# Kernel optimization log

Measured on AMD Instinct MI355X. Metric: run time of the kernel, lower is better.

The kernel has to match this reference:

```python
import jax, jax.numpy as jnp
import numpy as np

D = 128   # query_token_dim = tgt_token_dim = qk_dim = v_dim (code constraints)
NH = 8
HD = D // NH
SCALE = HD ** -0.5
B = 4096  # BH1W1: number of cost-map query locations
H0, W0 = 12, 18  # target token spatial size (H3, W3)


def _ln(x, g, b, eps=1e-5):
    m = x.mean(-1, keepdims=True)
    v = ((x - m) ** 2).mean(-1, keepdims=True)
    return (x - m) * jax.lax.rsqrt(v + eps) * g + b


def _broad_attn(q1, kw, vw):
    # q1: [D] single query broadcast across batch; kw, vw: [B, L, D]
    Bq, L, _ = kw.shape
    qh = q1.reshape(NH, HD)
    kh = kw.reshape(Bq, L, NH, HD)
    vh = vw.reshape(Bq, L, NH, HD)
    a = jax.nn.softmax(jnp.einsum('hd,blhd->bhl', qh, kh) * SCALE, axis=-1)
    return jnp.einsum('bhl,blhd->bhd', a, vh).reshape(Bq, D)


def _forward(query, tgt_token, ln1_g, ln1_b, ln2_g, ln2_b, wq, bq, wk, bk, wv, bv,
             wp, bp, f1w, f1b, f2w, f2b, cw, cb,
             ln1c_g, ln1c_b, ln2c_g, ln2c_b, wqc, bqc, wkc, bkc, wvc, bvc,
             wpc, bpc, f1cw, f1cb, f2cw, f2cb, H, W):
    Bq = tgt_token.shape[0]
    sc = query  # [1, 10, D]
    # ---- fine branch: 6 windows (2x3 grid) over full-res target tokens ----
    qn = _ln(query[:, :6, :], ln1_g, ln1_b)
    q = (qn @ wq + bq)[0]                                   # [6, D]
    k = (tgt_token @ wk + bk).reshape(Bq, H, W, D)
    v = (tgt_token @ wv + bv).reshape(Bq, H, W, D)
    hs = [(0, H // 2), (H // 2, H)]
    ws = [(0, W // 3), (W // 3, 2 * (W // 3)), (2 * (W // 3), W)]
    wins = [(h0, h1, w0, w1) for (h0, h1) in hs for (w0, w1) in ws]
    outs = [_broad_attn(q[i],
                        k[:, h0:h1, w0:w1].reshape(Bq, -1, D),
                        v[:, h0:h1, w0:w1].reshape(Bq, -1, D))
            for i, (h0, h1, w0, w1) in enumerate(wins)]
    x = jnp.stack(outs, axis=1)                             # [B, 6, D]
    x = sc[:, :6, :] + (x @ wp + bp)
    xn = _ln(x, ln2_g, ln2_b)
    x_fine = x + (jax.nn.gelu(xn @ f1w + f1b, approximate=False) @ f2w + f2b)
    # ---- coarse branch: 3x3/s2 conv downsample, 4 windows (2x2 grid) ----
    tc = jax.lax.conv_general_dilated(tgt_token.reshape(Bq, H, W, D), cw,
                                      (2, 2), ((1, 1), (1, 1)),
                                      dimension_numbers=('NHWC', 'HWIO', 'NHWC')) + cb
    Hc, Wc = tc.shape[1], tc.shape[2]
    qn = _ln(sc[:, 6:10, :], ln1c_g, ln1c_b)
    qc = (qn @ wqc + bqc)[0]                                # [4, D]
    kc = tc @ wkc + bkc
    vc = tc @ wvc + bvc
    hs = [(0, Hc // 2), (Hc // 2, Hc)]
    ws = [(0, Wc // 2), (Wc // 2, Wc)]
    wins = [(h0, h1, w0, w1) for (h0, h1) in hs for (w0, w1) in ws]
    outs = [_broad_attn(qc[i],
                        kc[:, h0:h1, w0:w1].reshape(Bq, -1, D),
                        vc[:, h0:h1, w0:w1].reshape(Bq, -1, D))
            for i, (h0, h1, w0, w1) in enumerate(wins)]
    x = jnp.stack(outs, axis=1)                             # [B, 4, D]
    x = sc[:, 6:10, :] + (x @ wpc + bpc)
    xn = _ln(x, ln2c_g, ln2c_b)
    x_coarse = x + (jax.nn.gelu(xn @ f1cw + f1cb, approximate=False) @ f2cw + f2cb)
    return jnp.concatenate([x_fine, x_coarse], axis=1)      # [B, 10, D]


def setup_inputs():
    key = jax.random.key(0)
    ks = jax.random.split(key, 16)
    def w(k, shape):
        return jax.random.normal(k, shape, jnp.float32) * 0.05
    z = jnp.zeros((D,), jnp.float32)
    o = jnp.ones((D,), jnp.float32)
    return dict(
        query=jax.random.normal(ks[0], (1, 10, D), jnp.float32),
        tgt_token=jax.random.normal(ks[1], (B, H0 * W0, D), jnp.float32),
        ln1_g=o, ln1_b=z, ln2_g=o, ln2_b=z,
        wq=w(ks[2], (D, D)), bq=z, wk=w(ks[3], (D, D)), bk=z,
        wv=w(ks[4], (D, D)), bv=z, wp=w(ks[5], (D, D)), bp=z,
        f1w=w(ks[6], (D, D)), f1b=z, f2w=w(ks[7], (D, D)), f2b=z,
        cw=w(ks[8], (3, 3, D, D)), cb=z,
        ln1c_g=o, ln1c_b=z, ln2c_g=o, ln2c_b=z,
        wqc=w(ks[9], (D, D)), bqc=z, wkc=w(ks[10], (D, D)), bkc=z,
        wvc=w(ks[11], (D, D)), bvc=z, wpc=w(ks[12], (D, D)), bpc=z,
        f1cw=w(ks[13], (D, D)), f1cb=z, f2cw=w(ks[14], (D, D)), f2cb=z,
        H=H0, W=W0,
    )


def reference(query, tgt_token, ln1_g, ln1_b, ln2_g, ln2_b, wq, bq, wk, bk, wv, bv,
              wp, bp, f1w, f1b, f2w, f2b, cw, cb,
              ln1c_g, ln1c_b, ln2c_g, ln2c_b, wqc, bqc, wkc, bkc, wvc, bvc,
              wpc, bpc, f1cw, f1cb, f2cw, f2cb, H, W):
    return _forward(query, tgt_token, ln1_g, ln1_b, ln2_g, ln2_b, wq, bq, wk, bk,
                    wv, bv, wp, bp, f1w, f1b, f2w, f2b, cw, cb,
                    ln1c_g, ln1c_b, ln2c_g, ln2c_b, wqc, bqc, wkc, bkc, wvc, bvc,
                    wpc, bpc, f1cw, f1cb, f2cw, f2cb, H, W)
```

## Files before the change

### kernel.cpp

```cpp
#include <hip/hip_runtime.h>
#include <math.h>


typedef short   mfrag  __attribute__((ext_vector_type(8)));
typedef float   floatx4 __attribute__((ext_vector_type(4)));
typedef unsigned short us4 __attribute__((ext_vector_type(4)));
typedef unsigned short us8 __attribute__((ext_vector_type(8)));
typedef unsigned int u32x4 __attribute__((ext_vector_type(4)));

#define LL   216
#define LC   54
#define TP1  136
#define TP2  72

__device__ __forceinline__ float b2f(unsigned short u){
  return __uint_as_float(((unsigned int)u) << 16);
}
__device__ __forceinline__ unsigned short f2b(float f){
  unsigned int x = __float_as_uint(f);
  return (unsigned short)((x + 0x7fffu + ((x >> 16) & 1u)) >> 16);
}
__device__ __forceinline__ floatx4 mfma16(mfrag a, mfrag b, floatx4 c){
  return __builtin_amdgcn_mfma_f32_16x16x32_bf16(a, b, c, 0, 0, 0);
}
__device__ __forceinline__ mfrag zfrag(){ mfrag z = {0,0,0,0,0,0,0,0}; return z; }

union F8 { unsigned short u[8]; mfrag v; };

struct Par {
  const float *query,*tgt,*ln1g,*ln1b,*ln2g,*ln2b,*wq,*bq,*wk,*wv,*bv,
              *wp,*bp,*f1w,*f1b,*f2w,*f2b,*cw,*cb;
  const float *ln1cg,*ln1cb,*ln2cg,*ln2cb,*wqc,*bqc,*wkc,*wvc,*bvc,
              *wpc,*bpc,*f1cw,*f1cb,*f2cw,*f2cb;
  unsigned short *U;
  float          *uc;
  float          *cvb;
  unsigned short *G;
  unsigned short *cwvT;
  unsigned short *wT;
  float          *out;
};

__global__ __launch_bounds__(256) void k0a(Par p){
  __shared__ float qn[10][128];
  __shared__ float qp[10][128];
  __shared__ unsigned short wkb[128*130];
  int tid = threadIdx.x;
  if (tid < 10){
    int r = tid;
    const float* row = p.query + r*128;
    float s1=0.f, s2=0.f;
    for (int c=0;c<128;c++){ float v=row[c]; s1+=v; s2+=v*v; }
    float m = s1/128.f, var = s2/128.f - m*m;
    float inv = rsqrtf(var + 1e-5f);
    const float* g  = (r<6)? p.ln1g : p.ln1cg;
    const float* bb = (r<6)? p.ln1b : p.ln1cb;
    for (int c=0;c<128;c++) qn[r][c] = (row[c]-m)*inv*g[c] + bb[c];
  }
  __syncthreads();
  for (int o=tid;o<1280;o+=256){
    int i=o>>7, d=o&127;
    const float* w  = (i<6)? p.wq : p.wqc;
    const float* bi = (i<6)? p.bq : p.bqc;
    float acc = bi[d];
    for (int c=0;c<128;c++) acc += qn[i][c]*w[c*128+d];
    qp[i][d]=acc;
  }
  if (tid < 128){
    int d = tid; float a = p.bvc[d];
    for (int c=0;c<128;c++) a += p.cb[c] * p.wvc[c*128+d];
    p.cvb[d] = a;
  }
  __syncthreads();
  for (int o=tid;o<16384;o+=256) wkb[(o>>7)*130 + (o&127)] = f2b(p.wk[o]);
  __syncthreads();
  for (int o=tid;o<6144;o+=256){
    int ih=o>>7, c=o&127, i=ih>>3, h=ih&7;
    float a=0.f;
    #pragma unroll
    for (int dd=0;dd<16;dd++) a += b2f(wkb[c*130 + h*16+dd]) * qp[i][h*16+dd];
    p.U[ih*128+c] = f2b(0.25f*a);
  }
  __syncthreads();
  for (int o=tid;o<16384;o+=256) wkb[(o>>7)*130 + (o&127)] = f2b(p.wkc[o]);
  __syncthreads();
  for (int o=tid;o<4096;o+=256){
    int ih=o>>7, c=o&127, i=ih>>3, h=ih&7;
    float a=0.f;
    #pragma unroll
    for (int dd=0;dd<16;dd++) a += b2f(wkb[c*130 + h*16+dd]) * qp[6+i][h*16+dd];
    p.uc[ih*128+c] = 0.25f*a;
  }
}

__global__ __launch_bounds__(256) void ktrans(Par p){
  __shared__ float lt[128*129];
  int bid = blockIdx.x, tid = threadIdx.x;
  const float* src;
  switch(bid){ case 0: src=p.wp;  break; case 1: src=p.f1w;  break;
               case 2: src=p.f2w; break; case 3: src=p.wpc;  break;
               case 4: src=p.f1cw;break; case 5: src=p.f2cw; break;
               case 6: src=p.wv;  break; default: src=p.wvc; }
  unsigned short* dst = p.wT + bid*16384;
  for (int o=tid;o<16384;o+=256){ int k=o>>7, n=o&127; lt[n*129+k] = src[o]; }
  __syncthreads();
  for (int o=tid;o<16384;o+=256){ int n=o>>7, k=o&127; dst[o] = f2b(lt[n*129+k]); }
}

__global__ __launch_bounds__(256) void kfold(Par p){
  __shared__ alignas(16) unsigned short cwb[128*136];
  __shared__ alignas(16) unsigned short ucb[32*136];
  int bid=blockIdx.x, tid=threadIdx.x;
  int lane=tid&63, w=tid>>6, q4=lane>>4, n16=lane&15;
  int tap = (bid<9)? bid : bid-9;
  for (int o=tid;o<16384;o+=256)
    cwb[(o>>7)*136 + (o&127)] = f2b(p.cw[(size_t)tap*16384 + o]);
  if (bid < 9){
    for (int o=tid;o<4096;o+=256) ucb[(o>>7)*136 + (o&127)] = f2b(p.uc[o]);
    __syncthreads();
    #pragma unroll
    for (int nt2=0;nt2<2;nt2++){
      int nt = w + nt2*4;
      #pragma unroll
      for (int mt=0;mt<2;mt++){
        floatx4 acc={0.f,0.f,0.f,0.f};
        #pragma unroll
        for (int ks=0;ks<4;ks++){
          mfrag a  = *reinterpret_cast<const mfrag*>(ucb + (mt*16+n16)*136 + ks*32+q4*8);
          mfrag bf = *reinterpret_cast<const mfrag*>(cwb + (nt*16+n16)*136 + ks*32+q4*8);
          acc = mfma16(a, bf, acc);
        }
        #pragma unroll
        for (int r=0;r<4;r++){
          int ih = mt*16+q4*4+r, e = nt*16+n16;
          p.G[(tap*32+ih)*128 + e] = f2b(acc[r]);
        }
      }
    }
  } else {
    __syncthreads();
    const unsigned short* wvcT = p.wT + 7*16384;
    #pragma unroll 1
    for (int mt=0;mt<8;mt++){
      #pragma unroll
      for (int nt2=0;nt2<2;nt2++){
        int nt = w + nt2*4;
        floatx4 acc={0.f,0.f,0.f,0.f};
        #pragma unroll
        for (int ks=0;ks<4;ks++){
          mfrag a  = *reinterpret_cast<const mfrag*>(cwb + (mt*16+n16)*136 + ks*32+q4*8);
          mfrag bf = *reinterpret_cast<const mfrag*>(wvcT + (nt*16+n16)*128 + ks*32+q4*8);
          acc = mfma16(a, bf, acc);
        }
        us4 pk = { f2b(acc[0]), f2b(acc[1]), f2b(acc[2]), f2b(acc[3]) };
        *reinterpret_cast<us4*>(p.cwvT + ((size_t)tap*128 + nt*16+n16)*128 + mt*16 + q4*4) = pk;
      }
    }
  }
}

__global__ __launch_bounds__(512, 4) void kmain(Par p){
  __shared__ __align__(16) unsigned char smem[79488];
  unsigned short* tile  = (unsigned short*)smem;
  unsigned short* rmap  = (unsigned short*)(smem + 55552);
  unsigned short* rmapF = (unsigned short*)(smem + 56704);
  unsigned char*  regn  = smem + 57472;
  float*          sfT   = (float*)regn;
  unsigned short* aw    = (unsigned short*)(regn + 13056);
  unsigned short* rbA   = (unsigned short*)regn;
  float*          sctT  = (float*)(regn + 13056);
  unsigned short* ac    = (unsigned short*)regn;
  unsigned short* rt0   = (unsigned short*)(regn + 4608);
  unsigned short* rt1   = (unsigned short*)(regn + 13312);

  int tid  = threadIdx.x;
  int b    = blockIdx.x;
  int lane = tid & 63, wvx = tid >> 6;
  int q4   = lane >> 4, n16 = lane & 15;
  const float* tb = p.tgt + (size_t)b*LL*128;
  const unsigned char* tB = (const unsigned char*)tile;

  auto tfragX = [&](unsigned ax, int kb)->mfrag {
    return *reinterpret_cast<const mfrag*>(
        tB + ((ax ^ (unsigned)(kb & 0x70)) + (unsigned)(kb & 0xFFFFFF8F)));
  };

  {
    int c4 = tid & 31;
    unsigned c8m = (unsigned)((c4*8) & 0x70), c8l = (unsigned)((c4*8) & 0x88);
    for (int o = tid; o < 217*32; o += 512){
      int row = o >> 5;
      float4 v = make_float4(0.f,0.f,0.f,0.f);
      if (row < 216) v = *reinterpret_cast<const float4*>(tb + row*128 + (c4<<2));
      us4 wv4 = { f2b(v.x), f2b(v.y), f2b(v.z), f2b(v.w) };
      unsigned s = (unsigned)((row & 7) << 4);
      unsigned addr = (unsigned)(row*256) + ((c8m ^ s) + c8l);
      *reinterpret_cast<us4*>((unsigned char*)tile + addr) = wv4;
    }
  }
  for (int o = tid; o < 960; o += 512){
    int row;
    if (o < 576){
      int tap = o >> 6, pos = o & 63;
      int ip = pos/9, jp = pos - ip*9;
      int r = ip*2 + tap/3 - 1, c = jp*2 + (tap%3) - 1;
      row = (pos < 54 && r >= 0 && r < 12 && c >= 0 && c < 18) ? (r*18 + c) : 216;
      rmap[o] = (unsigned short)(row*256 + ((row&7)<<4));
    } else {
      int t = o - 576; int win = t >> 6, lw = t & 63;
      int r0 = (win/3)*6, c0 = (win%3)*6;
      row = (lw < 36) ? ((r0 + lw/6)*18 + c0 + lw%6) : 216;
      rmapF[t] = (unsigned short)(row*256 + ((row&7)<<4));
    }
  }
  __syncthreads();

  for (int task = wvx; task < 18; task += 8){
    int win = task/3, rg = task - win*3;
    unsigned ax = rmapF[win*64 + rg*16 + n16];
    floatx4 acc = {0.f,0.f,0.f,0.f};
    #pragma unroll
    for (int ks=0; ks<4; ks++){
      mfrag a = tfragX(ax, ks*64 + q4*16);
      mfrag bf = zfrag();
      if (n16 < 8) bf = *reinterpret_cast<const mfrag*>(p.U + (win*8+n16)*128 + ks*32 + q4*8);
      acc = mfma16(a, bf, acc);
    }
    if (n16 < 8){
      #pragma unroll
      for (int r=0;r<4;r++){
        int l = rg*16 + q4*4 + r;
        if (l < 36) sfT[(win*8+n16)*40 + l] = acc[r];
      }
    }
  }
  __syncthreads();
  {
    int l = lane;
    for (int rr=0; rr<6; rr++){
      int row = wvx*6 + rr;
      float v = (l < 36) ? sfT[row*40 + l] : -1e30f;
      float mx = v;
      #pragma unroll
      for (int m=1;m<64;m<<=1) mx = fmaxf(mx, __shfl_xor(mx, m));
      float e = (l < 36) ? __expf(v - mx) : 0.f;
      float sm = e;
      #pragma unroll
      for (int m=1;m<64;m<<=1) sm += __shfl_xor(sm, m);
      aw[row*TP2 + l] = f2b(e * (1.f/sm));
    }
  }
  __syncthreads();
  {
    int nt = wvx;
    unsigned c2 = (unsigned)((nt*16 + n16)*2);
    unsigned c2m = c2 & 0x70u, c2l = c2 & 0x8Fu;
    for (int win=0; win<6; win++){
      floatx4 acc={0.f,0.f,0.f,0.f};
      #pragma unroll
      for (int ks=0; ks<2; ks++){
        mfrag a = zfrag();
        if (n16 < 8) a = *reinterpret_cast<const mfrag*>(aw + (win*8+n16)*TP2 + ks*32 + q4*8);
        us8 rv = *reinterpret_cast<const us8*>(rmapF + win*64 + ks*32 + q4*8);
        F8 bb;
        #pragma unroll
        for (int j=0;j<8;j++)
          bb.u[j] = *reinterpret_cast<const unsigned short*>(tB + (((unsigned)rv[j] ^ c2m) + c2l));
        acc = mfma16(a, bb.v, acc);
      }
      #pragma unroll
      for (int r=0;r<4;r++){
        int h = q4*4 + r;
        if (h < 8) rbA[(win*8+h)*TP1 + nt*16 + n16] = f2b(acc[r]);
      }
    }
  }
  __syncthreads();
  {
    int h = wvx;
    const unsigned short* wvT = p.wT + 6*16384;
    floatx4 acc = {0.f,0.f,0.f,0.f};
    #pragma unroll
    for (int ks=0; ks<4; ks++){
      mfrag a = zfrag();
      if (n16 < 6) a = *reinterpret_cast<const mfrag*>(rbA + (n16*8+h)*TP1 + ks*32 + q4*8);
      mfrag bf = *reinterpret_cast<const mfrag*>(wvT + (h*16+n16)*128 + ks*32 + q4*8);
      acc = mfma16(a, bf, acc);
    }
    float bvd = p.bv[h*16+n16];
    #pragma unroll
    for (int r=0;r<4;r++){
      int win = q4*4 + r;
      if (win < 6) p.out[((size_t)b*10 + win)*128 + h*16 + n16] = acc[r] + bvd;
    }
  }
  {
    int g = wvx >> 1, nt = wvx & 1;
    int pos = g*16 + n16;
    floatx4 acc = {0.f,0.f,0.f,0.f};
    for (int tap=0; tap<9; tap++){
      unsigned ax = rmap[tap*64 + pos];
      #pragma unroll
      for (int ks=0; ks<4; ks++){
        mfrag a = tfragX(ax, ks*64 + q4*16);
        mfrag bf = *reinterpret_cast<const mfrag*>(
            p.G + (size_t)(tap*32 + nt*16 + n16)*128 + ks*32 + q4*8);
        acc = mfma16(a, bf, acc);
      }
    }
    #pragma unroll
    for (int r=0;r<4;r++){
      int l = g*16 + q4*4 + r;
      if (l < LC) sctT[(nt*16+n16)*56 + l] = acc[r];
    }
  }
  __syncthreads();
  {
    int l = lane;
    int rl = (l < 54) ? (l/9) : 0, cl = (l < 54) ? (l - (l/9)*9) : 0;
    for (int rr=0; rr<4; rr++){
      int ih = wvx*4 + rr;
      int i = ih >> 3;
      int rA = (i>>1)*3, cA = (i&1)*4, cB = (i&1)? 9 : 4;
      bool member = (l < 54) && rl >= rA && rl < rA+3 && cl >= cA && cl < cB;
      float s = member ? sctT[ih*56 + l] : -1e30f;
      float mx = s;
      #pragma unroll
      for (int m=1;m<64;m<<=1) mx = fmaxf(mx, __shfl_xor(mx, m));
      float e = member ? __expf(s - mx) : 0.f;
      float sm = e;
      #pragma unroll
      for (int m=1;m<64;m<<=1) sm += __shfl_xor(sm, m);
      ac[ih*TP2 + l] = f2b(e * (1.f/sm));
    }
  }
  __syncthreads();
  {
    floatx4 pacc = {0.f,0.f,0.f,0.f};
    int h = wvx, nt = wvx;
    unsigned c2 = (unsigned)((nt*16 + n16)*2);
    unsigned c2m = c2 & 0x70u, c2l = c2 & 0x8Fu;
    for (int tap=0; tap<9; tap++){
      unsigned short* rtw = (tap & 1) ? rt1 : rt0;
      us8 rv0 = *reinterpret_cast<const us8*>(rmap + tap*64 +      q4*8);
      us8 rv1 = *reinterpret_cast<const us8*>(rmap + tap*64 + 32 + q4*8);
      F8 b0, b1;
      #pragma unroll
      for (int j=0;j<8;j++){
        b0.u[j] = *reinterpret_cast<const unsigned short*>(tB + (((unsigned)rv0[j] ^ c2m) + c2l));
        b1.u[j] = *reinterpret_cast<const unsigned short*>(tB + (((unsigned)rv1[j] ^ c2m) + c2l));
      }
      #pragma unroll
      for (int mt=0; mt<2; mt++){
        mfrag a0 = *reinterpret_cast<const mfrag*>(ac + (mt*16+n16)*TP2 +      q4*8);
        mfrag a1 = *reinterpret_cast<const mfrag*>(ac + (mt*16+n16)*TP2 + 32 + q4*8);
        floatx4 rr = {0.f,0.f,0.f,0.f};
        rr = mfma16(a0, b0.v, rr);
        rr = mfma16(a1, b1.v, rr);
        #pragma unroll
        for (int r=0;r<4;r++){
          int ih = mt*16 + q4*4 + r;
          rtw[ih*TP1 + nt*16 + n16] = f2b(rr[r]);
        }
      }
      __syncthreads();
      #pragma unroll
      for (int ks=0; ks<4; ks++){
        mfrag a = zfrag();
        if (n16 < 4) a = *reinterpret_cast<const mfrag*>(rtw + (n16*8 + h)*TP1 + ks*32 + q4*8);
        mfrag bf = *reinterpret_cast<const mfrag*>(
            p.cwvT + ((size_t)tap*128 + h*16 + n16)*128 + ks*32 + q4*8);
        pacc = mfma16(a, bf, pacc);
      }
    }
    if (q4 == 0){
      #pragma unroll
      for (int r=0;r<4;r++){
        int d = h*16 + n16;
        p.out[((size_t)b*10 + 6 + r)*128 + d] = pacc[r] + p.cvb[d];
      }
    }
  }
}

__global__ __launch_bounds__(256) void kffn(Par p){
  __shared__ alignas(16) unsigned short ba[64*TP1];
  __shared__ alignas(16) unsigned short bbq[64*TP1];
  __shared__ alignas(16) unsigned short xb[64*TP1];
  int tid=threadIdx.x, bid=blockIdx.x;
  int lane=tid&63, wvv=tid>>6, q4=lane>>4, n16=lane&15;
  bool fine = bid < 384;
  int rows0 = fine? bid*64 : (bid-384)*64;
  int TPB = fine? 6 : 4, toff = fine? 0 : 6;
  const unsigned short* w1 = p.wT + (fine?0:3)*16384;
  const unsigned short* w2 = p.wT + (fine?1:4)*16384;
  const unsigned short* w3 = p.wT + (fine?2:5)*16384;
  const float* bi1 = fine? p.bp  : p.bpc;
  const float* bi2 = fine? p.f1b : p.f1cb;
  const float* bi3 = fine? p.f2b : p.f2cb;
  const float* g2  = fine? p.ln2g : p.ln2cg;
  const float* be2 = fine? p.ln2b : p.ln2cb;

  for (int ci=tid; ci<64*32; ci+=256){
    int row=ci>>5, c4=ci&31;
    int grow = rows0 + row;
    int bglob = grow / TPB, t = toff + (grow % TPB);
    float4 v = *reinterpret_cast<const float4*>(p.out + ((size_t)bglob*10+t)*128 + c4*4);
    us4 o = { f2b(v.x), f2b(v.y), f2b(v.z), f2b(v.w) };
    *reinterpret_cast<us4*>(ba + row*TP1 + c4*4) = o;
  }
  __syncthreads();
  {
    mfrag A[4];
    #pragma unroll
    for (int ks=0;ks<4;ks++) A[ks] = *reinterpret_cast<const mfrag*>(ba + (wvv*16+n16)*TP1 + ks*32+q4*8);
    for (int nt=0;nt<8;nt++){
      floatx4 acc={0.f,0.f,0.f,0.f};
      #pragma unroll
      for (int ks=0;ks<4;ks++){
        mfrag Bf = *reinterpret_cast<const mfrag*>(w1 + (nt*16+n16)*128 + ks*32+q4*8);
        acc = mfma16(A[ks], Bf, acc);
      }
      #pragma unroll
      for (int r=0;r<4;r++){
        int row = wvv*16+q4*4+r;
        int grow = rows0 + row;
        int t = toff + (grow % TPB);
        int d = nt*16+n16;
        xb[row*TP1+d] = f2b(acc[r] + bi1[d] + p.query[t*128+d]);
      }
    }
  }
  __syncthreads();
  {
    float ga = g2[lane], gb = g2[64+lane];
    float ea = be2[lane], eb = be2[64+lane];
    for (int rr=0; rr<16; rr++){
      int row = wvv*16 + rr;
      float v0 = b2f(xb[row*TP1 + lane]);
      float v1 = b2f(xb[row*TP1 + 64 + lane]);
      float s = v0+v1, sq = v0*v0+v1*v1;
      #pragma unroll
      for (int m=1;m<64;m<<=1){ s += __shfl_xor(s, m); sq += __shfl_xor(sq, m); }
      float mean = s*(1.f/128.f), var = sq*(1.f/128.f) - mean*mean;
      float inv = rsqrtf(var + 1e-5f);
      bbq[row*TP1 + lane]      = f2b((v0-mean)*inv*ga + ea);
      bbq[row*TP1 + 64 + lane] = f2b((v1-mean)*inv*gb + eb);
    }
  }
  __syncthreads();
  {
    mfrag A[4];
    #pragma unroll
    for (int ks=0;ks<4;ks++) A[ks] = *reinterpret_cast<const mfrag*>(bbq + (wvv*16+n16)*TP1 + ks*32+q4*8);
    for (int nt=0;nt<8;nt++){
      floatx4 acc={0.f,0.f,0.f,0.f};
      #pragma unroll
      for (int ks=0;ks<4;ks++){
        mfrag Bf = *reinterpret_cast<const mfrag*>(w2 + (nt*16+n16)*128 + ks*32+q4*8);
        acc = mfma16(A[ks], Bf, acc);
      }
      #pragma unroll
      for (int r=0;r<4;r++){
        int row=wvv*16+q4*4+r, d=nt*16+n16;
        float v = acc[r] + bi2[d];
        ba[row*TP1+d] = f2b(0.5f*v*(1.f+erff(v*0.70710678118f)));
      }
    }
  }
  __syncthreads();
  {
    mfrag A[4];
    #pragma unroll
    for (int ks=0;ks<4;ks++) A[ks] = *reinterpret_cast<const mfrag*>(ba + (wvv*16+n16)*TP1 + ks*32+q4*8);
    for (int nt=0;nt<8;nt++){
      floatx4 acc={0.f,0.f,0.f,0.f};
      #pragma unroll
      for (int ks=0;ks<4;ks++){
        mfrag Bf = *reinterpret_cast<const mfrag*>(w3 + (nt*16+n16)*128 + ks*32+q4*8);
        acc = mfma16(A[ks], Bf, acc);
      }
      #pragma unroll
      for (int r=0;r<4;r++){
        int row=wvv*16+q4*4+r, d=nt*16+n16;
        int grow=rows0+row;
        int bglob = grow / TPB, t = toff + (grow % TPB);
        p.out[((size_t)bglob*10+t)*128+d] = b2f(xb[row*TP1+d]) + acc[r] + bi3[d];
      }
    }
  }
}

extern "C" void kernel_launch(void* const* d_in, const int* in_sizes, int n_in,
                              void* d_out, int out_size, void* d_ws, size_t ws_size,
                              hipStream_t stream){
  (void)in_sizes; (void)n_in; (void)out_size; (void)ws_size;
  Par p;
  p.query=(const float*)d_in[0];  p.tgt  =(const float*)d_in[1];
  p.ln1g =(const float*)d_in[2];  p.ln1b =(const float*)d_in[3];
  p.ln2g =(const float*)d_in[4];  p.ln2b =(const float*)d_in[5];
  p.wq   =(const float*)d_in[6];  p.bq   =(const float*)d_in[7];
  p.wk   =(const float*)d_in[8];
  p.wv   =(const float*)d_in[10]; p.bv   =(const float*)d_in[11];
  p.wp   =(const float*)d_in[12]; p.bp   =(const float*)d_in[13];
  p.f1w  =(const float*)d_in[14]; p.f1b  =(const float*)d_in[15];
  p.f2w  =(const float*)d_in[16]; p.f2b  =(const float*)d_in[17];
  p.cw   =(const float*)d_in[18]; p.cb   =(const float*)d_in[19];
  p.ln1cg=(const float*)d_in[20]; p.ln1cb=(const float*)d_in[21];
  p.ln2cg=(const float*)d_in[22]; p.ln2cb=(const float*)d_in[23];
  p.wqc  =(const float*)d_in[24]; p.bqc  =(const float*)d_in[25];
  p.wkc  =(const float*)d_in[26];
  p.wvc  =(const float*)d_in[28]; p.bvc  =(const float*)d_in[29];
  p.wpc  =(const float*)d_in[30]; p.bpc  =(const float*)d_in[31];
  p.f1cw =(const float*)d_in[32]; p.f1cb =(const float*)d_in[33];
  p.f2cw =(const float*)d_in[34]; p.f2cb =(const float*)d_in[35];
  char* ws = (char*)d_ws;
  p.U    = (unsigned short*)(ws + 0);
  p.uc   = (float*)        (ws + 16384);
  p.cvb  = (float*)        (ws + 32768);
  p.G    = (unsigned short*)(ws + 33280);
  p.cwvT = (unsigned short*)(ws + 107008);
  p.wT   = (unsigned short*)(ws + 401920);
  p.out  = (float*)d_out;

  k0a   <<<dim3(1),    dim3(256), 0, stream>>>(p);
  ktrans<<<dim3(8),    dim3(256), 0, stream>>>(p);
  kfold <<<dim3(18),   dim3(256), 0, stream>>>(p);
  kmain <<<dim3(4096), dim3(512), 0, stream>>>(p);
  kffn  <<<dim3(640),  dim3(256), 0, stream>>>(p);
}
```

Baseline: 1.099 ms.

## Fuse FFN epilogue into main kernel and restructure coarse value projection

Removes the separate kffn kernel and runs the projection, LayerNorm, GELU MLP and residual for all 10 query tokens per batch element inside kmain, keeping intermediates in shared memory instead of round-tripping through the output buffer. The coarse branch now computes conv-folded values for all 64 positions as an MFMA GEMM into a swizzled LDS tile, then does a single attention-weighted reduction, replacing the per-tap loop with 9 barriers. The weight transpose kernel is merged into the prep kernel to cut one launch. The trade-off is that each block runs small, mostly padded MFMAs (only 6 or 10 of 16 rows used) and uses slightly more LDS, which may limit occupancy.

```diff
diff --git a/kernel.cpp b/kernel.cpp
--- a/kernel.cpp
+++ b/kernel.cpp
@@ -6,7 +6,6 @@
 typedef float   floatx4 __attribute__((ext_vector_type(4)));
 typedef unsigned short us4 __attribute__((ext_vector_type(4)));
 typedef unsigned short us8 __attribute__((ext_vector_type(8)));
-typedef unsigned int u32x4 __attribute__((ext_vector_type(4)));
 
 #define LL   216
 #define LC   54
@@ -41,11 +40,26 @@
   float          *out;
 };
 
-__global__ __launch_bounds__(256) void k0a(Par p){
-  __shared__ float qn[10][128];
-  __shared__ float qp[10][128];
-  __shared__ unsigned short wkb[128*130];
-  int tid = threadIdx.x;
+__global__ __launch_bounds__(256) void kprep(Par p){
+  __shared__ __align__(16) unsigned char sm[66048];
+  int bid = blockIdx.x, tid = threadIdx.x;
+  if (bid > 0){
+    float* lt = (float*)sm;
+    int slot = bid - 1;
+    const float* src;
+    switch(slot){ case 0: src=p.wp;  break; case 1: src=p.f1w;  break;
+                  case 2: src=p.f2w; break; case 3: src=p.wpc;  break;
+                  case 4: src=p.f1cw;break; case 5: src=p.f2cw; break;
+                  case 6: src=p.wv;  break; default: src=p.wvc; }
+    unsigned short* dst = p.wT + slot*16384;
+    for (int o=tid;o<16384;o+=256){ int k=o>>7, n=o&127; lt[n*129+k] = src[o]; }
+    __syncthreads();
+    for (int o=tid;o<16384;o+=256){ int n=o>>7, k=o&127; dst[o] = f2b(lt[n*129+k]); }
+    return;
+  }
+  float* qn = (float*)sm;
+  float* qp = (float*)(sm + 5120);
+  unsigned short* wkb = (unsigned short*)(sm + 10240);
   if (tid < 10){
     int r = tid;
     const float* row = p.query + r*128;
@@ -55,7 +69,7 @@
     float inv = rsqrtf(var + 1e-5f);
     const float* g  = (r<6)? p.ln1g : p.ln1cg;
     const float* bb = (r<6)? p.ln1b : p.ln1cb;
-    for (int c=0;c<128;c++) qn[r][c] = (row[c]-m)*inv*g[c] + bb[c];
+    for (int c=0;c<128;c++) qn[r*128+c] = (row[c]-m)*inv*g[c] + bb[c];
   }
   __syncthreads();
   for (int o=tid;o<1280;o+=256){
@@ -63,8 +77,8 @@
     const float* w  = (i<6)? p.wq : p.wqc;
     const float* bi = (i<6)? p.bq : p.bqc;
     float acc = bi[d];
-    for (int c=0;c<128;c++) acc += qn[i][c]*w[c*128+d];
-    qp[i][d]=acc;
+    for (int c=0;c<128;c++) acc += qn[i*128+c]*w[c*128+d];
+    qp[i*128+d]=acc;
   }
   if (tid < 128){
     int d = tid; float a = p.bvc[d];
@@ -78,7 +92,7 @@
     int ih=o>>7, c=o&127, i=ih>>3, h=ih&7;
     float a=0.f;
     #pragma unroll
-    for (int dd=0;dd<16;dd++) a += b2f(wkb[c*130 + h*16+dd]) * qp[i][h*16+dd];
+    for (int dd=0;dd<16;dd++) a += b2f(wkb[c*130 + h*16+dd]) * qp[i*128 + h*16+dd];
     p.U[ih*128+c] = f2b(0.25f*a);
   }
   __syncthreads();
@@ -88,23 +102,9 @@
     int ih=o>>7, c=o&127, i=ih>>3, h=ih&7;
     float a=0.f;
     #pragma unroll
-    for (int dd=0;dd<16;dd++) a += b2f(wkb[c*130 + h*16+dd]) * qp[6+i][h*16+dd];
+    for (int dd=0;dd<16;dd++) a += b2f(wkb[c*130 + h*16+dd]) * qp[(6+i)*128 + h*16+dd];
     p.uc[ih*128+c] = 0.25f*a;
   }
-}
-
-__global__ __launch_bounds__(256) void ktrans(Par p){
-  __shared__ float lt[128*129];
-  int bid = blockIdx.x, tid = threadIdx.x;
-  const float* src;
-  switch(bid){ case 0: src=p.wp;  break; case 1: src=p.f1w;  break;
-               case 2: src=p.f2w; break; case 3: src=p.wpc;  break;
-               case 4: src=p.f1cw;break; case 5: src=p.f2cw; break;
-               case 6: src=p.wv;  break; default: src=p.wvc; }
-  unsigned short* dst = p.wT + bid*16384;
-  for (int o=tid;o<16384;o+=256){ int k=o>>7, n=o&127; lt[n*129+k] = src[o]; }
-  __syncthreads();
-  for (int o=tid;o<16384;o+=256){ int n=o>>7, k=o&127; dst[o] = f2b(lt[n*129+k]); }
 }
 
 __global__ __launch_bounds__(256) void kfold(Par p){
@@ -160,7 +160,7 @@
 }
 
 __global__ __launch_bounds__(512, 4) void kmain(Par p){
-  __shared__ __align__(16) unsigned char smem[79488];
+  __shared__ __align__(16) unsigned char smem[81184];
   unsigned short* tile  = (unsigned short*)smem;
   unsigned short* rmap  = (unsigned short*)(smem + 55552);
   unsigned short* rmapF = (unsigned short*)(smem + 56704);
@@ -169,9 +169,12 @@
   unsigned short* aw    = (unsigned short*)(regn + 13056);
   unsigned short* rbA   = (unsigned short*)regn;
   float*          sctT  = (float*)(regn + 13056);
+  unsigned short* ba    = (unsigned short*)(regn + 20992);
   unsigned short* ac    = (unsigned short*)regn;
-  unsigned short* rt0   = (unsigned short*)(regn + 4608);
-  unsigned short* rt1   = (unsigned short*)(regn + 13312);
+  unsigned char*  vcT   = regn + 4608;
+  unsigned short* xb    = (unsigned short*)regn;
+  unsigned short* bbq   = (unsigned short*)(regn + 2720);
+  unsigned short* hb    = (unsigned short*)(regn + 5440);
 
   int tid  = threadIdx.x;
   int b    = blockIdx.x;
@@ -291,7 +294,7 @@
     #pragma unroll
     for (int r=0;r<4;r++){
       int win = q4*4 + r;
-      if (win < 6) p.out[((size_t)b*10 + win)*128 + h*16 + n16] = acc[r] + bvd;
+      if (win < 6) ba[win*TP1 + h*16 + n16] = f2b(acc[r] + bvd);
     }
   }
   {
@@ -336,156 +339,144 @@
   }
   __syncthreads();
   {
-    floatx4 pacc = {0.f,0.f,0.f,0.f};
-    int h = wvx, nt = wvx;
-    unsigned c2 = (unsigned)((nt*16 + n16)*2);
-    unsigned c2m = c2 & 0x70u, c2l = c2 & 0x8Fu;
+    int dt = wvx;
+    floatx4 va0={0.f,0.f,0.f,0.f}, va1={0.f,0.f,0.f,0.f},
+            va2={0.f,0.f,0.f,0.f}, va3={0.f,0.f,0.f,0.f};
     for (int tap=0; tap<9; tap++){
-      unsigned short* rtw = (tap & 1) ? rt1 : rt0;
-      us8 rv0 = *reinterpret_cast<const us8*>(rmap + tap*64 +      q4*8);
-      us8 rv1 = *reinterpret_cast<const us8*>(rmap + tap*64 + 32 + q4*8);
-      F8 b0, b1;
-      #pragma unroll
-      for (int j=0;j<8;j++){
-        b0.u[j] = *reinterpret_cast<const unsigned short*>(tB + (((unsigned)rv0[j] ^ c2m) + c2l));
-        b1.u[j] = *reinterpret_cast<const unsigned short*>(tB + (((unsigned)rv1[j] ^ c2m) + c2l));
-      }
-      #pragma unroll
-      for (int mt=0; mt<2; mt++){
-        mfrag a0 = *reinterpret_cast<const mfrag*>(ac + (mt*16+n16)*TP2 +      q4*8);
-        mfrag a1 = *reinterpret_cast<const mfrag*>(ac + (mt*16+n16)*TP2 + 32 + q4*8);
-        floatx4 rr = {0.f,0.f,0.f,0.f};
-        rr = mfma16(a0, b0.v, rr);
-        rr = mfma16(a1, b1.v, rr);
-        #pragma unroll
-        for (int r=0;r<4;r++){
-          int ih = mt*16 + q4*4 + r;
-          rtw[ih*TP1 + nt*16 + n16] = f2b(rr[r]);
-        }
-      }
-      __syncthreads();
+      unsigned ax0 = rmap[tap*64 +  0 + n16];
+      unsigned ax1 = rmap[tap*64 + 16 + n16];
+      unsigned ax2 = rmap[tap*64 + 32 + n16];
+      unsigned ax3 = rmap[tap*64 + 48 + n16];
+      const unsigned short* cwp = p.cwvT + ((size_t)tap*128 + dt*16 + n16)*128;
       #pragma unroll
       for (int ks=0; ks<4; ks++){
-        mfrag a = zfrag();
-        if (n16 < 4) a = *reinterpret_cast<const mfrag*>(rtw + (n16*8 + h)*TP1 + ks*32 + q4*8);
-        mfrag bf = *reinterpret_cast<const mfrag*>(
-            p.cwvT + ((size_t)tap*128 + h*16 + n16)*128 + ks*32 + q4*8);
-        pacc = mfma16(a, bf, pacc);
-      }
-    }
-    if (q4 == 0){
-      #pragma unroll
-      for (int r=0;r<4;r++){
-        int d = h*16 + n16;
-        p.out[((size_t)b*10 + 6 + r)*128 + d] = pacc[r] + p.cvb[d];
-      }
-    }
-  }
-}
-
-__global__ __launch_bounds__(256) void kffn(Par p){
-  __shared__ alignas(16) unsigned short ba[64*TP1];
-  __shared__ alignas(16) unsigned short bbq[64*TP1];
-  __shared__ alignas(16) unsigned short xb[64*TP1];
-  int tid=threadIdx.x, bid=blockIdx.x;
-  int lane=tid&63, wvv=tid>>6, q4=lane>>4, n16=lane&15;
-  bool fine = bid < 384;
-  int rows0 = fine? bid*64 : (bid-384)*64;
-  int TPB = fine? 6 : 4, toff = fine? 0 : 6;
-  const unsigned short* w1 = p.wT + (fine?0:3)*16384;
-  const unsigned short* w2 = p.wT + (fine?1:4)*16384;
-  const unsigned short* w3 = p.wT + (fine?2:5)*16384;
-  const float* bi1 = fine? p.bp  : p.bpc;
-  const float* bi2 = fine? p.f1b : p.f1cb;
-  const float* bi3 = fine? p.f2b : p.f2cb;
-  const float* g2  = fine? p.ln2g : p.ln2cg;
-  const float* be2 = fine? p.ln2b : p.ln2cb;
-
-  for (int ci=tid; ci<64*32; ci+=256){
-    int row=ci>>5, c4=ci&31;
-    int grow = rows0 + row;
-    int bglob = grow / TPB, t = toff + (grow % TPB);
-    float4 v = *reinterpret_cast<const float4*>(p.out + ((size_t)bglob*10+t)*128 + c4*4);
-    us4 o = { f2b(v.x), f2b(v.y), f2b(v.z), f2b(v.w) };
-    *reinterpret_cast<us4*>(ba + row*TP1 + c4*4) = o;
-  }
-  __syncthreads();
-  {
-    mfrag A[4];
-    #pragma unroll
-    for (int ks=0;ks<4;ks++) A[ks] = *reinterpret_cast<const mfrag*>(ba + (wvv*16+n16)*TP1 + ks*32+q4*8);
-    for (int nt=0;nt<8;nt++){
-      floatx4 acc={0.f,0.f,0.f,0.f};
-      #pragma unroll
-      for (int ks=0;ks<4;ks++){
-        mfrag Bf = *reinterpret_cast<const mfrag*>(w1 + (nt*16+n16)*128 + ks*32+q4*8);
-        acc = mfma16(A[ks], Bf, acc);
-      }
-      #pragma unroll
-      for (int r=0;r<4;r++){
-        int row = wvv*16+q4*4+r;
-        int grow = rows0 + row;
-        int t = toff + (grow % TPB);
-        int d = nt*16+n16;
-        xb[row*TP1+d] = f2b(acc[r] + bi1[d] + p.query[t*128+d]);
-      }
-    }
-  }
-  __syncthreads();
-  {
-    float ga = g2[lane], gb = g2[64+lane];
-    float ea = be2[lane], eb = be2[64+lane];
-    for (int rr=0; rr<16; rr++){
-      int row = wvv*16 + rr;
-      float v0 = b2f(xb[row*TP1 + lane]);
-      float v1 = b2f(xb[row*TP1 + 64 + lane]);
-      float s = v0+v1, sq = v0*v0+v1*v1;
-      #pragma unroll
-      for (int m=1;m<64;m<<=1){ s += __shfl_xor(s, m); sq += __shfl_xor(sq, m); }
-      float mean = s*(1.f/128.f), var = sq*(1.f/128.f) - mean*mean;
-      float inv = rsqrtf(var + 1e-5f);
-      bbq[row*TP1 + lane]      = f2b((v0-mean)*inv*ga + ea);
-      bbq[row*TP1 + 64 + lane] = f2b((v1-mean)*inv*gb + eb);
-    }
-  }
-  __syncthreads();
-  {
-    mfrag A[4];
-    #pragma unroll
-    for (int ks=0;ks<4;ks++) A[ks] = *reinterpret_cast<const mfrag*>(bbq + (wvv*16+n16)*TP1 + ks*32+q4*8);
-    for (int nt=0;nt<8;nt++){
-      floatx4 acc={0.f,0.f,0.f,0.f};
-      #pragma unroll
-      for (int ks=0;ks<4;ks++){
-        mfrag Bf = *reinterpret_cast<const mfrag*>(w2 + (nt*16+n16)*128 + ks*32+q4*8);
-        acc = mfma16(A[ks], Bf, acc);
-      }
-      #pragma unroll
-      for (int r=0;r<4;r++){
-        int row=wvv*16+q4*4+r, d=nt*16+n16;
-        float v = acc[r] + bi2[d];
-        ba[row*TP1+d] = f2b(0.5f*v*(1.f+erff(v*0.70710678118f)));
-      }
-    }
-  }
-  __syncthreads();
-  {
-    mfrag A[4];
-    #pragma unroll
-    for (int ks=0;ks<4;ks++) A[ks] = *reinterpret_cast<const mfrag*>(ba + (wvv*16+n16)*TP1 + ks*32+q4*8);
-    for (int nt=0;nt<8;nt++){
-      floatx4 acc={0.f,0.f,0.f,0.f};
-      #pragma unroll
-      for (int ks=0;ks<4;ks++){
-        mfrag Bf = *reinterpret_cast<const mfrag*>(w3 + (nt*16+n16)*128 + ks*32+q4*8);
-        acc = mfma16(A[ks], Bf, acc);
-      }
-      #pragma unroll
-      for (int r=0;r<4;r++){
-        int row=wvv*16+q4*4+r, d=nt*16+n16;
-        int grow=rows0+row;
-        int bglob = grow / TPB, t = toff + (grow % TPB);
-        p.out[((size_t)bglob*10+t)*128+d] = b2f(xb[row*TP1+d]) + acc[r] + bi3[d];
+        mfrag bf = *reinterpret_cast<const mfrag*>(cwp + ks*32 + q4*8);
+        va0 = mfma16(tfragX(ax0, ks*64 + q4*16), bf, va0);
+        va1 = mfma16(tfragX(ax1, ks*64 + q4*16), bf, va1);
+        va2 = mfma16(tfragX(ax2, ks*64 + q4*16), bf, va2);
+        va3 = mfma16(tfragX(ax3, ks*64 + q4*16), bf, va3);
+      }
+    }
+    int d = dt*16 + n16;
+    unsigned drow = (unsigned)(d*128), dsw = (unsigned)((d & 7) << 4);
+    us4 p0 = { f2b(va0[0]), f2b(va0[1]), f2b(va0[2]), f2b(va0[3]) };
+    us4 p1 = { f2b(va1[0]), f2b(va1[1]), f2b(va1[2]), f2b(va1[3]) };
+    us4 p2 = { f2b(va2[0]), f2b(va2[1]), f2b(va2[2]), f2b(va2[3]) };
+    us4 p3 = { f2b(va3[0]), f2b(va3[1]), f2b(va3[2]), f2b(va3[3]) };
+    *reinterpret_cast<us4*>(vcT + drow + ((unsigned)( 0 + q4*8) ^ dsw)) = p0;
+    *reinterpret_cast<us4*>(vcT + drow + ((unsigned)(32 + q4*8) ^ dsw)) = p1;
+    *reinterpret_cast<us4*>(vcT + drow + ((unsigned)(64 + q4*8) ^ dsw)) = p2;
+    *reinterpret_cast<us4*>(vcT + drow + ((unsigned)(96 + q4*8) ^ dsw)) = p3;
+  }
+  __syncthreads();
+  {
+    int nt = wvx, d = nt*16 + n16;
+    unsigned dsw = (unsigned)((d & 7) << 4);
+    floatx4 pa0={0.f,0.f,0.f,0.f}, pa1={0.f,0.f,0.f,0.f};
+    #pragma unroll
+    for (int ks=0; ks<2; ks++){
+      mfrag bf = *reinterpret_cast<const mfrag*>(
+          vcT + (unsigned)(d*128) + ((unsigned)(ks*64 + q4*16) ^ dsw));
+      mfrag a0 = *reinterpret_cast<const mfrag*>(ac + n16*TP2        + ks*32 + q4*8);
+      mfrag a1 = *reinterpret_cast<const mfrag*>(ac + (16+n16)*TP2   + ks*32 + q4*8);
+      pa0 = mfma16(a0, bf, pa0);
+      pa1 = mfma16(a1, bf, pa1);
+    }
+    float cvbd = p.cvb[d];
+    float s0 = 0.f, s1 = 0.f;
+    #pragma unroll
+    for (int r=0;r<4;r++) if ((nt&3)==r){ s0 = pa0[r]; s1 = pa1[r]; }
+    int q_lo = nt>>2, q_hi = q_lo + 2;
+    if (q4 == q_lo){ ba[6*TP1 + d] = f2b(s0 + cvbd); ba[8*TP1 + d] = f2b(s1 + cvbd); }
+    if (q4 == q_hi){ ba[7*TP1 + d] = f2b(s0 + cvbd); ba[9*TP1 + d] = f2b(s1 + cvbd); }
+  }
+  __syncthreads();
+  {
+    int nt = wvx, d = nt*16 + n16;
+    const unsigned short* wF = p.wT + 0*16384;
+    const unsigned short* wC = p.wT + 3*16384;
+    floatx4 aF={0.f,0.f,0.f,0.f}, aC={0.f,0.f,0.f,0.f};
+    #pragma unroll
+    for (int ks=0;ks<4;ks++){
+      mfrag vF = zfrag(), vC = zfrag();
+      if (n16 < 6)       vF = *reinterpret_cast<const mfrag*>(ba + n16*TP1 + ks*32+q4*8);
+      else if (n16 < 10) vC = *reinterpret_cast<const mfrag*>(ba + n16*TP1 + ks*32+q4*8);
+      mfrag BF = *reinterpret_cast<const mfrag*>(wF + (nt*16+n16)*128 + ks*32+q4*8);
+      mfrag BC = *reinterpret_cast<const mfrag*>(wC + (nt*16+n16)*128 + ks*32+q4*8);
+      aF = mfma16(vF, BF, aF);
+      aC = mfma16(vC, BC, aC);
+    }
+    float bF = p.bp[d], bC = p.bpc[d];
+    #pragma unroll
+    for (int r=0;r<4;r++){
+      int m = q4*4+r;
+      if (m < 6)            xb[m*TP1+d] = f2b(aF[r] + bF + p.query[m*128+d]);
+      else if (m < 10)      xb[m*TP1+d] = f2b(aC[r] + bC + p.query[m*128+d]);
+    }
+  }
+  __syncthreads();
+  for (int row = wvx; row < 10; row += 8){
+    bool fine = row < 6;
+    const float* g2 = fine? p.ln2g : p.ln2cg;
+    const float* e2 = fine? p.ln2b : p.ln2cb;
+    float v0 = b2f(xb[row*TP1 + lane]), v1 = b2f(xb[row*TP1 + 64 + lane]);
+    float s = v0+v1, sq = v0*v0+v1*v1;
+    #pragma unroll
+    for (int m=1;m<64;m<<=1){ s += __shfl_xor(s, m); sq += __shfl_xor(sq, m); }
+    float mean = s*(1.f/128.f), var = sq*(1.f/128.f) - mean*mean;
+    float inv = rsqrtf(var + 1e-5f);
+    bbq[row*TP1 + lane]      = f2b((v0-mean)*inv*g2[lane] + e2[lane]);
+    bbq[row*TP1 + 64 + lane] = f2b((v1-mean)*inv*g2[64+lane] + e2[64+lane]);
+  }
+  __syncthreads();
+  {
+    int nt = wvx, d = nt*16 + n16;
+    const unsigned short* wF = p.wT + 1*16384;
+    const unsigned short* wC = p.wT + 4*16384;
+    floatx4 aF={0.f,0.f,0.f,0.f}, aC={0.f,0.f,0.f,0.f};
+    #pragma unroll
+    for (int ks=0;ks<4;ks++){
+      mfrag vF = zfrag(), vC = zfrag();
+      if (n16 < 6)       vF = *reinterpret_cast<const mfrag*>(bbq + n16*TP1 + ks*32+q4*8);
+      else if (n16 < 10) vC = *reinterpret_cast<const mfrag*>(bbq + n16*TP1 + ks*32+q4*8);
+      mfrag BF = *reinterpret_cast<const mfrag*>(wF + (nt*16+n16)*128 + ks*32+q4*8);
+      mfrag BC = *reinterpret_cast<const mfrag*>(wC + (nt*16+n16)*128 + ks*32+q4*8);
+      aF = mfma16(vF, BF, aF);
+      aC = mfma16(vC, BC, aC);
+    }
+    float bF = p.f1b[d], bC = p.f1cb[d];
+    #pragma unroll
+    for (int r=0;r<4;r++){
+      int m = q4*4+r;
+      float v;
+      if (m < 6) v = aF[r] + bF;
+      else       v = aC[r] + bC;
+      if (m < 10) hb[m*TP1+d] = f2b(0.5f*v*(1.f+erff(v*0.70710678118f)));
+    }
+  }
+  __syncthreads();
+  {
+    int nt = wvx, d = nt*16 + n16;
+    const unsigned short* wF = p.wT + 2*16384;
+    const unsigned short* wC = p.wT + 5*16384;
+    floatx4 aF={0.f,0.f,0.f,0.f}, aC={0.f,0.f,0.f,0.f};
+    #pragma unroll
+    for (int ks=0;ks<4;ks++){
+      mfrag vF = zfrag(), vC = zfrag();
+      if (n16 < 6)       vF = *reinterpret_cast<const mfrag*>(hb + n16*TP1 + ks*32+q4*8);
+      else if (n16 < 10) vC = *reinterpret_cast<const mfrag*>(hb + n16*TP1 + ks*32+q4*8);
+      mfrag BF = *reinterpret_cast<const mfrag*>(wF + (nt*16+n16)*128 + ks*32+q4*8);
+      mfrag BC = *reinterpret_cast<const mfrag*>(wC + (nt*16+n16)*128 + ks*32+q4*8);
+      aF = mfma16(vF, BF, aF);
+      aC = mfma16(vC, BC, aC);
+    }
+    float bF = p.f2b[d], bC = p.f2cb[d];
+    #pragma unroll
+    for (int r=0;r<4;r++){
+      int m = q4*4+r;
+      if (m < 10){
+        float accv = (m < 6) ? (aF[r] + bF) : (aC[r] + bC);
+        p.out[((size_t)b*10 + m)*128 + d] = b2f(xb[m*TP1+d]) + accv;
       }
     }
   }
@@ -523,9 +514,7 @@
   p.wT   = (unsigned short*)(ws + 401920);
   p.out  = (float*)d_out;
 
-  k0a   <<<dim3(1),    dim3(256), 0, stream>>>(p);
-  ktrans<<<dim3(8),    dim3(256), 0, stream>>>(p);
-  kfold <<<dim3(18),   dim3(256), 0, stream>>>(p);
-  kmain <<<dim3(4096), dim3(512), 0, stream>>>(p);
-  kffn  <<<dim3(640),  dim3(256), 0, stream>>>(p);
-}
+  kprep<<<dim3(9),    dim3(256), 0, stream>>>(p);
+  kfold<<<dim3(18),   dim3(256), 0, stream>>>(p);
+  kmain<<<dim3(4096), dim3(512), 0, stream>>>(p);
+}
```

Result: no change. 1.113 ms (+1.3%).
